# Optimization experiments

Hardware: AMD Instinct MI355X
Metric: run time of the kernel (lower is better)

## Reference

```python
import jax, jax.numpy as jnp
import numpy as np

B, S, H = 128, 1000, 256


def setup_inputs() -> dict:
    key = jax.random.key(0)
    ks = jax.random.split(key, 15)
    sc = 1.0 / np.sqrt(H)
    f = lambda k, shape: (jax.random.normal(k, shape, jnp.float32) * sc)
    return dict(
        static_hidden=jax.random.normal(ks[0], (B, S, H), jnp.float32),
        state_embedding=jax.random.normal(ks[1], (B, 1, H), jnp.float32),
        decoder_hidden=jax.random.normal(ks[2], (B, 1, H), jnp.float32),
        target_hidden=jax.random.normal(ks[3], (B, 1, H), jnp.float32),
        last_hh=jax.random.normal(ks[4], (1, B, H), jnp.float32),
        W_ih=f(ks[5], (3 * H, H)),
        W_hh=f(ks[6], (3 * H, H)),
        b_ih=f(ks[7], (3 * H,)),
        b_hh=f(ks[8], (3 * H,)),
        v_attn_enc=f(ks[9], (H,)),
        W_attn_enc=f(ks[10], (H, 2 * H)),
        v_attn_tgt=f(ks[11], (H,)),
        W_attn_tgt=f(ks[12], (H, 2 * H)),
        v_ptr=f(ks[13], (H,)),
        W_ptr=f(ks[14], (H, 3 * H)),
    )


def _attention(static, dec, v, W):
    # static: [B,S,H], dec: [B,1,H] -> softmax attention over S
    hid = jnp.concatenate([static, jnp.broadcast_to(dec, static.shape)], axis=2)  # [B,S,2H]
    t = jnp.tanh(jnp.einsum('hk,bsk->bhs', W, hid))  # [B,H,S]
    return jax.nn.softmax(jnp.einsum('h,bhs->bs', v, t), axis=1)  # [B,S]


def _gru_step(x, h, Wih, Whh, bih, bhh):
    # single-layer single-step torch GRU semantics; x,h: [B,H]
    gi = x @ Wih.T + bih
    gh = h @ Whh.T + bhh
    ir, iz, ig = jnp.split(gi, 3, axis=-1)
    hr, hz, hg = jnp.split(gh, 3, axis=-1)
    r = jax.nn.sigmoid(ir + hr)
    z = jax.nn.sigmoid(iz + hz)
    n = jnp.tanh(ig + r * hg)
    return (1.0 - z) * n + z * h


def _pointer_branch(static, state_emb, attn, v, W):
    context = jnp.einsum('bs,bsh->bh', attn, static)[:, None, :]  # [B,1,H]
    energy = jnp.concatenate(
        [static,
         jnp.broadcast_to(context, static.shape),
         jnp.broadcast_to(state_emb, static.shape)], axis=2)  # [B,S,3H]
    return jnp.einsum('h,bhs->bs', v, jnp.tanh(jnp.einsum('hk,bsk->bhs', W, energy)))


def reference(static_hidden, state_embedding, decoder_hidden, target_hidden, last_hh,
              W_ih, W_hh, b_ih, b_hh,
              v_attn_enc, W_attn_enc, v_attn_tgt, W_attn_tgt, v_ptr, W_ptr):
    # GRU step (dropout is identity in eval / p=0.0)
    h_new = _gru_step(decoder_hidden[:, 0, :], last_hh[0], W_ih, W_hh, b_ih, b_hh)
    rnn_out = h_new[:, None, :]  # [B,1,H]
    last_hh_new = h_new[None]    # [1,B,H]

    enc_attn = _attention(static_hidden, rnn_out, v_attn_enc, W_attn_enc)
    probs = _pointer_branch(static_hidden, state_embedding, enc_attn, v_ptr, W_ptr)

    tgt_attn = _attention(static_hidden, target_hidden, v_attn_tgt, W_attn_tgt)
    # NOTE: original code reuses self.v / self.W (not v_target/W_taret) for the
    # target branch energy -- replicated faithfully.
    probs_target = _pointer_branch(static_hidden, state_embedding, tgt_attn, v_ptr, W_ptr)

    return (5.0 * probs + probs_target, last_hh_new)
```

## Files before the change

kernel.cpp:

```cpp
#include <hip/hip_runtime.h>
#include <hip/hip_bf16.h>
#include <stdint.h>
#include <stddef.h>

#define Bn 128
#define Sn 1000
#define SP 1024
#define Hn 256

typedef __bf16 bf16;
typedef __bf16 bf16x8 __attribute__((ext_vector_type(8)));
typedef __bf16 bf16x4 __attribute__((ext_vector_type(4)));
typedef __bf16 bf16x2 __attribute__((ext_vector_type(2)));
typedef float  f32x4  __attribute__((ext_vector_type(4)));

typedef __attribute__((address_space(1))) const unsigned int* gas1;
typedef __attribute__((address_space(3))) unsigned int* las3;

__device__ __forceinline__ float fast_tanh(float x){
  return 1.0f - 2.0f / (__expf(2.0f * x) + 1.0f);
}
__device__ __forceinline__ float fast_sigmoid(float x){
  return 1.0f / (1.0f + __expf(-x));
}
__device__ __forceinline__ float dot4(float4 a, float4 b){
  return a.x*b.x + a.y*b.y + a.z*b.z + a.w*b.w;
}

__global__ void k0a_convert(const float* __restrict__ stat, bf16* __restrict__ Abf){
  int p = blockIdx.x * 256 + threadIdx.x;
  int row = p >> 5;
  int ch  = p & 31;
  int s = row & (SP - 1);
  int b = row >> 10;
  float4 f0 = make_float4(0.f,0.f,0.f,0.f), f1 = f0;
  if (s < Sn){
    const float4* src = (const float4*)(stat + ((size_t)(b*Sn + s))*Hn + ch*8);
    f0 = src[0]; f1 = src[1];
  }
  bf16x8 v;
  v[0]=(bf16)f0.x; v[1]=(bf16)f0.y; v[2]=(bf16)f0.z; v[3]=(bf16)f0.w;
  v[4]=(bf16)f1.x; v[5]=(bf16)f1.y; v[6]=(bf16)f1.z; v[7]=(bf16)f1.w;
  *(bf16x8*)(Abf + (size_t)row*Hn + ch*8) = v;
}

__global__ void k0b_weights(const float* __restrict__ We, const float* __restrict__ Wt,
                            const float* __restrict__ Wp, bf16* __restrict__ Wcb,
                            float* __restrict__ sc_e, float* __restrict__ sc_t){
  int t = blockIdx.x * 256 + threadIdx.x;
  if (t < Bn * SP) { sc_e[t] = 0.f; sc_t[t] = 0.f; }
  int r = t >> 8, c = t & 255;
  float val;
  if (r < 256)       val = We[r*512 + c];
  else if (r < 512)  val = Wt[(r-256)*512 + c];
  else               val = Wp[(r-512)*768 + c];
  Wcb[t] = (bf16)val;
}

__global__ void k1_gru(const float* __restrict__ dec, const float* __restrict__ lhh,
                       const float* __restrict__ tgt, const float* __restrict__ se,
                       const float* __restrict__ Wih, const float* __restrict__ Whh,
                       const float* __restrict__ bih, const float* __restrict__ bhh,
                       const float* __restrict__ We,  const float* __restrict__ Wt,
                       const float* __restrict__ Wp,
                       float* __restrict__ out_hh, float* __restrict__ d_enc,
                       float* __restrict__ d_tgt,  float* __restrict__ c3){
  __shared__ __align__(16) float xs[256], hs[256], hn[256], ts[256], ss[256];
  int b = blockIdx.x, t = threadIdx.x;
  xs[t] = dec[b*256 + t];
  hs[t] = lhh[b*256 + t];
  ts[t] = tgt[b*256 + t];
  ss[t] = se[b*256 + t];
  __syncthreads();

  const float4* wir = (const float4*)(Wih + (size_t)t*256);
  const float4* wiz = (const float4*)(Wih + (size_t)(256+t)*256);
  const float4* wig = (const float4*)(Wih + (size_t)(512+t)*256);
  const float4* whr = (const float4*)(Whh + (size_t)t*256);
  const float4* whz = (const float4*)(Whh + (size_t)(256+t)*256);
  const float4* whg = (const float4*)(Whh + (size_t)(512+t)*256);
  float gir=0.f, giz=0.f, gig=0.f, ghr=0.f, ghz=0.f, ghg=0.f;
  #pragma unroll 4
  for (int k=0;k<64;k++){
    float4 xv = ((const float4*)xs)[k];
    float4 hv = ((const float4*)hs)[k];
    gir += dot4(wir[k], xv);
    giz += dot4(wiz[k], xv);
    gig += dot4(wig[k], xv);
    ghr += dot4(whr[k], hv);
    ghz += dot4(whz[k], hv);
    ghg += dot4(whg[k], hv);
  }
  gir += bih[t];      ghr += bhh[t];
  giz += bih[256+t];  ghz += bhh[256+t];
  gig += bih[512+t];  ghg += bhh[512+t];
  float r = fast_sigmoid(gir + ghr);
  float z = fast_sigmoid(giz + ghz);
  float n = fast_tanh(gig + r*ghg);
  float h = (1.f - z)*n + z*hs[t];
  hn[t] = h;
  out_hh[b*256 + t] = h;
  __syncthreads();

  const float4* we2 = (const float4*)(We + (size_t)t*512 + 256);
  const float4* wt2 = (const float4*)(Wt + (size_t)t*512 + 256);
  const float4* wp3 = (const float4*)(Wp + (size_t)t*768 + 512);
  float de=0.f, dt=0.f, cv=0.f;
  #pragma unroll 4
  for (int k=0;k<64;k++){
    float4 hv = ((const float4*)hn)[k];
    float4 tv = ((const float4*)ts)[k];
    float4 sv = ((const float4*)ss)[k];
    de += dot4(we2[k], hv);
    dt += dot4(wt2[k], tv);
    cv += dot4(wp3[k], sv);
  }
  d_enc[b*256 + t] = de;
  d_tgt[b*256 + t] = dt;
  c3[b*256 + t]    = cv;
}

__global__ __launch_bounds__(256) void k2_gemm(
    const bf16* __restrict__ Abf, const bf16* __restrict__ Wcb,
    const float* __restrict__ d_enc, const float* __restrict__ d_tgt,
    const float* __restrict__ c3, const float* __restrict__ v_enc,
    const float* __restrict__ v_tgt,
    float* __restrict__ sc_e, float* __restrict__ sc_t,
    bf16* __restrict__ Aptr){
  __shared__ __align__(16) bf16 As[128*64];
  __shared__ __align__(16) bf16 Bs[128*64];
  int tid = threadIdx.x;
  int w = tid >> 6, l = tid & 63;
  int nc = blockIdx.x, st = blockIdx.y, b = blockIdx.z;
  int wm = (w >> 1) * 64, wn = (w & 1) * 64;
  int lm = l & 15, q = l >> 4;

  const bf16* gA = Abf + (size_t)(b*SP + st*128) * Hn;
  const bf16* gB = Wcb + (size_t)(nc*128) * Hn;
  int srow = w*8 + (l >> 3);
  int scol = (l & 7) * 8;

  f32x4 acc[4][4];
  #pragma unroll
  for (int i=0;i<4;i++)
    #pragma unroll
    for (int j=0;j<4;j++) acc[i][j] = (f32x4){0.f,0.f,0.f,0.f};

  for (int kt=0; kt<4; ++kt){
    __syncthreads();
    #pragma unroll
    for (int r=0;r<4;r++){
      int rowg = r*32 + srow;
      __builtin_amdgcn_global_load_lds((gas1)(gA + (size_t)rowg*Hn + kt*64 + scol),
                                       (las3)(&As[(r*32 + w*8)*64]), 16, 0, 0);
      __builtin_amdgcn_global_load_lds((gas1)(gB + (size_t)rowg*Hn + kt*64 + scol),
                                       (las3)(&Bs[(r*32 + w*8)*64]), 16, 0, 0);
    }
    __syncthreads();
    const bf16* Ab = &As[(wm + lm)*64 + q*8];
    const bf16* Bb = &Bs[(wn + lm)*64 + q*8];
    #pragma unroll
    for (int kk=0; kk<64; kk+=32){
      bf16x8 af[4], bfr[4];
      #pragma unroll
      for (int i=0;i<4;i++) af[i]  = *(const bf16x8*)(Ab + i*16*64 + kk);
      #pragma unroll
      for (int j=0;j<4;j++) bfr[j] = *(const bf16x8*)(Bb + j*16*64 + kk);
      #pragma unroll
      for (int i=0;i<4;i++)
        #pragma unroll
        for (int j=0;j<4;j++)
          acc[i][j] = __builtin_amdgcn_mfma_f32_16x16x32_bf16(af[i], bfr[j], acc[i][j], 0, 0, 0);
    }
  }

  int hb = (nc & 1) * 128;
  if (nc < 4){
    const float* vv = (nc < 2) ? v_enc : v_tgt;
    const float* db = ((nc < 2) ? d_enc : d_tgt) + b*256;
    float* sc = ((nc < 2) ? sc_e : sc_t) + b*SP + st*128;
    float vj[4], dj[4];
    #pragma unroll
    for (int j=0;j<4;j++){
      int hh = hb + wn + j*16 + lm;
      vj[j] = vv[hh]; dj[j] = db[hh];
    }
    #pragma unroll
    for (int i=0;i<4;i++){
      #pragma unroll
      for (int r=0;r<4;r++){
        float p = 0.f;
        #pragma unroll
        for (int j=0;j<4;j++) p += vj[j] * fast_tanh(acc[i][j][r] + dj[j]);
        p += __shfl_xor(p, 1);
        p += __shfl_xor(p, 2);
        p += __shfl_xor(p, 4);
        p += __shfl_xor(p, 8);
        if (lm == 0) atomicAdd(&sc[wm + i*16 + q*4 + r], p);
      }
    }
  } else {
    const float* c3b = c3 + b*256;
    size_t rbase = (size_t)(b*SP + st*128);
    #pragma unroll
    for (int j=0;j<4;j++){
      int hh = hb + wn + j*16 + lm;
      float cv = c3b[hh];
      #pragma unroll
      for (int i=0;i<4;i++){
        #pragma unroll
        for (int r=0;r<4;r++){
          int row = wm + i*16 + q*4 + r;
          Aptr[(rbase + row)*Hn + hh] = (bf16)(acc[i][j][r] + cv);
        }
      }
    }
  }
}

__global__ void k3_softmax_ctx(const float* __restrict__ sc_e, const float* __restrict__ sc_t,
                               const bf16* __restrict__ Abf, const float* __restrict__ Wp,
                               float* __restrict__ c2e, float* __restrict__ c2t){
  int b = blockIdx.x, which = blockIdx.y, t = threadIdx.x;
  const float* sc = which ? sc_t : sc_e;
  float* c2 = which ? c2t : c2e;
  __shared__ __align__(16) float at[Sn];
  __shared__ float red[256];
  __shared__ __align__(16) float ctx[256];
  __shared__ float2 partc[2][128];

  float lmax = -1e30f;
  #pragma unroll
  for (int i=0;i<4;i++){
    int s = t + i*256;
    if (s < Sn){ float v = sc[b*SP + s]; at[s] = v; lmax = fmaxf(lmax, v); }
  }
  red[t] = lmax; __syncthreads();
  for (int o=128;o>0;o>>=1){ if (t < o) red[t] = fmaxf(red[t], red[t+o]); __syncthreads(); }
  float mx = red[0]; __syncthreads();

  float lsum = 0.f;
  #pragma unroll
  for (int i=0;i<4;i++){
    int s = t + i*256;
    if (s < Sn){ float e = __expf(at[s] - mx); at[s] = e; lsum += e; }
  }
  red[t] = lsum; __syncthreads();
  for (int o=128;o>0;o>>=1){ if (t < o) red[t] += red[t+o]; __syncthreads(); }
  float inv = 1.0f / red[0];
  #pragma unroll
  for (int i=0;i<4;i++){
    int s = t + i*256;
    if (s < Sn) at[s] *= inv;
  }
  __syncthreads();

  int hp = t & 127, sh = t >> 7;
  float a0 = 0.f, a1 = 0.f;
  const bf16* base = Abf + ((size_t)(b*SP + sh*500))*Hn + hp*2;
  #pragma unroll 4
  for (int s2=0; s2<500; s2++){
    float wgt = at[sh*500 + s2];
    bf16x2 pr = *(const bf16x2*)(base + (size_t)s2*Hn);
    a0 += wgt * (float)pr[0];
    a1 += wgt * (float)pr[1];
  }
  partc[sh][hp] = make_float2(a0, a1);
  __syncthreads();
  if (t < 128){
    float2 p0 = partc[0][t], p1 = partc[1][t];
    ctx[2*t]   = p0.x + p1.x;
    ctx[2*t+1] = p0.y + p1.y;
  }
  __syncthreads();

  const float4* wrow = (const float4*)(Wp + (size_t)t*768 + 256);
  float acc = 0.f;
  #pragma unroll 4
  for (int k=0;k<64;k++) acc += dot4(wrow[k], ((const float4*)ctx)[k]);
  c2[b*256 + t] = acc;
}

__global__ void k4_final(const bf16* __restrict__ Aptr, const float* __restrict__ c2e,
                         const float* __restrict__ c2t, const float* __restrict__ vp,
                         float* __restrict__ out){
  int w = threadIdx.x >> 6, l = threadIdx.x & 63;
  int row = blockIdx.x*4 + w;
  int b = row / 1000;
  int s = row - b*1000;
  const bf16* ap = Aptr + ((size_t)(b*SP + s))*Hn + l*4;
  bf16x4 av = *(const bf16x4*)ap;
  float4 ce = *(const float4*)(c2e + b*256 + l*4);
  float4 ct = *(const float4*)(c2t + b*256 + l*4);
  float4 vv = *(const float4*)(vp + l*4);
  float a0 = (float)av[0], a1 = (float)av[1], a2 = (float)av[2], a3 = (float)av[3];
  float pe = vv.x*fast_tanh(a0+ce.x) + vv.y*fast_tanh(a1+ce.y)
           + vv.z*fast_tanh(a2+ce.z) + vv.w*fast_tanh(a3+ce.w);
  float pt = vv.x*fast_tanh(a0+ct.x) + vv.y*fast_tanh(a1+ct.y)
           + vv.z*fast_tanh(a2+ct.z) + vv.w*fast_tanh(a3+ct.w);
  #pragma unroll
  for (int o=1;o<64;o<<=1){
    pe += __shfl_xor(pe, o);
    pt += __shfl_xor(pt, o);
  }
  if (l == 0) out[row] = 5.0f*pe + pt;
}

extern "C" void kernel_launch(void* const* d_in, const int* in_sizes, int n_in,
                              void* d_out, int out_size, void* d_ws, size_t ws_size,
                              hipStream_t stream){
  const float* stat = (const float*)d_in[0];
  const float* se   = (const float*)d_in[1];
  const float* dec  = (const float*)d_in[2];
  const float* tgt  = (const float*)d_in[3];
  const float* lhh  = (const float*)d_in[4];
  const float* Wih  = (const float*)d_in[5];
  const float* Whh  = (const float*)d_in[6];
  const float* bih  = (const float*)d_in[7];
  const float* bhh  = (const float*)d_in[8];
  const float* vEnc = (const float*)d_in[9];
  const float* WEnc = (const float*)d_in[10];
  const float* vTgt = (const float*)d_in[11];
  const float* WTgt = (const float*)d_in[12];
  const float* vPtr = (const float*)d_in[13];
  const float* WPtr = (const float*)d_in[14];
  float* out = (float*)d_out;

  char* wsp = (char*)d_ws;
  bf16*  Abf  = (bf16*)(wsp);
  bf16*  Aptr = (bf16*)(wsp + 67108864);
  bf16*  Wcb  = (bf16*)(wsp + 134217728);
  float* scE  = (float*)(wsp + 134610944);
  float* scT  = (float*)(wsp + 135135232);
  float* dEnc = (float*)(wsp + 135659520);
  float* dTgt = (float*)(wsp + 135790592);
  float* c3   = (float*)(wsp + 135921664);
  float* c2e  = (float*)(wsp + 136052736);
  float* c2t  = (float*)(wsp + 136183808);

  hipLaunchKernelGGL(k0a_convert, dim3(16384), dim3(256), 0, stream, stat, Abf);
  hipLaunchKernelGGL(k0b_weights, dim3(768), dim3(256), 0, stream,
                     WEnc, WTgt, WPtr, Wcb, scE, scT);
  hipLaunchKernelGGL(k1_gru, dim3(128), dim3(256), 0, stream,
                     dec, lhh, tgt, se, Wih, Whh, bih, bhh, WEnc, WTgt, WPtr,
                     out + Bn*Sn, dEnc, dTgt, c3);
  hipLaunchKernelGGL(k2_gemm, dim3(6, 8, 128), dim3(256), 0, stream,
                     Abf, Wcb, dEnc, dTgt, c3, vEnc, vTgt, scE, scT, Aptr);
  hipLaunchKernelGGL(k3_softmax_ctx, dim3(128, 2), dim3(256), 0, stream,
                     scE, scT, Abf, WPtr, c2e, c2t);
  hipLaunchKernelGGL(k4_final, dim3(32000), dim3(256), 0, stream,
                     Aptr, c2e, c2t, vPtr, out);
}
```

Baseline: 511.2 us.

## Keep A tile resident across all weight chunks and split softmax-context kernel

```diff
diff --git a/kernel.cpp b/kernel.cpp
--- a/kernel.cpp
+++ b/kernel.cpp
@@ -45,10 +45,8 @@
 }
 
 __global__ void k0b_weights(const float* __restrict__ We, const float* __restrict__ Wt,
-                            const float* __restrict__ Wp, bf16* __restrict__ Wcb,
-                            float* __restrict__ sc_e, float* __restrict__ sc_t){
+                            const float* __restrict__ Wp, bf16* __restrict__ Wcb){
   int t = blockIdx.x * 256 + threadIdx.x;
-  if (t < Bn * SP) { sc_e[t] = 0.f; sc_t[t] = 0.f; }
   int r = t >> 8, c = t & 255;
   float val;
   if (r < 256)       val = We[r*512 + c];
@@ -127,158 +125,210 @@
     const float* __restrict__ v_tgt,
     float* __restrict__ sc_e, float* __restrict__ sc_t,
     bf16* __restrict__ Aptr){
-  __shared__ __align__(16) bf16 As[128*64];
+  __shared__ __align__(16) bf16 As[64*256];
   __shared__ __align__(16) bf16 Bs[128*64];
+  __shared__ float scoreE[64], scoreT[64];
   int tid = threadIdx.x;
   int w = tid >> 6, l = tid & 63;
-  int nc = blockIdx.x, st = blockIdx.y, b = blockIdx.z;
-  int wm = (w >> 1) * 64, wn = (w & 1) * 64;
+  int st = blockIdx.x, b = blockIdx.y;
+  int wm = (w & 1) * 32, wn = (w >> 1) * 64;
   int lm = l & 15, q = l >> 4;
 
-  const bf16* gA = Abf + (size_t)(b*SP + st*128) * Hn;
-  const bf16* gB = Wcb + (size_t)(nc*128) * Hn;
-  int srow = w*8 + (l >> 3);
-  int scol = (l & 7) * 8;
-
-  f32x4 acc[4][4];
-  #pragma unroll
-  for (int i=0;i<4;i++)
+  if (tid < 64) scoreE[tid] = 0.f;
+  else if (tid < 128) scoreT[tid-64] = 0.f;
+
+  {
+    const bf16* gA = Abf + ((size_t)(b*SP + st*64)) * Hn;
+    int rl = w*2 + (l >> 5);
+    int ch = l & 31;
     #pragma unroll
-    for (int j=0;j<4;j++) acc[i][j] = (f32x4){0.f,0.f,0.f,0.f};
-
-  for (int kt=0; kt<4; ++kt){
-    __syncthreads();
+    for (int is = 0; is < 8; is++){
+      int row = is*8 + rl;
+      int sc_ = ch ^ (row & 7);
+      __builtin_amdgcn_global_load_lds((gas1)(gA + (size_t)row*256 + sc_*8),
+                                       (las3)(&As[(is*8 + w*2)*256]), 16, 0, 0);
+    }
+  }
+
+  int rB8 = w*8 + (l >> 3);
+  int chB = l & 7;
+
+  for (int nc = 0; nc < 6; nc++){
+    f32x4 acc[2][4];
     #pragma unroll
-    for (int r=0;r<4;r++){
-      int rowg = r*32 + srow;
-      __builtin_amdgcn_global_load_lds((gas1)(gA + (size_t)rowg*Hn + kt*64 + scol),
-                                       (las3)(&As[(r*32 + w*8)*64]), 16, 0, 0);
-      __builtin_amdgcn_global_load_lds((gas1)(gB + (size_t)rowg*Hn + kt*64 + scol),
-                                       (las3)(&Bs[(r*32 + w*8)*64]), 16, 0, 0);
+    for (int i=0;i<2;i++)
+      #pragma unroll
+      for (int j=0;j<4;j++) acc[i][j] = (f32x4){0.f,0.f,0.f,0.f};
+
+    for (int kt = 0; kt < 4; kt++){
+      __syncthreads();
+      #pragma unroll
+      for (int is = 0; is < 4; is++){
+        int row = is*32 + rB8;
+        int sc_ = chB ^ (row & 7);
+        __builtin_amdgcn_global_load_lds((gas1)(Wcb + ((size_t)(nc*128 + row))*256 + kt*64 + sc_*8),
+                                         (las3)(&Bs[(is*32 + w*8)*64]), 16, 0, 0);
+      }
+      __syncthreads();
+      #pragma unroll
+      for (int kk = 0; kk < 64; kk += 32){
+        bf16x8 af[2], bfr[4];
+        int cA = kt*8 + (kk >> 3) + q;
+        int cB = (kk >> 3) + q;
+        #pragma unroll
+        for (int i=0;i<2;i++){
+          int rA = wm + i*16 + lm;
+          af[i] = *(const bf16x8*)(&As[rA*256 + ((cA ^ (rA & 7)) << 3)]);
+        }
+        #pragma unroll
+        for (int j=0;j<4;j++){
+          int rB = wn + j*16 + lm;
+          bfr[j] = *(const bf16x8*)(&Bs[rB*64 + ((cB ^ (rB & 7)) << 3)]);
+        }
+        #pragma unroll
+        for (int i=0;i<2;i++)
+          #pragma unroll
+          for (int j=0;j<4;j++)
+            acc[i][j] = __builtin_amdgcn_mfma_f32_16x16x32_bf16(af[i], bfr[j], acc[i][j], 0, 0, 0);
+      }
     }
-    __syncthreads();
-    const bf16* Ab = &As[(wm + lm)*64 + q*8];
-    const bf16* Bb = &Bs[(wn + lm)*64 + q*8];
-    #pragma unroll
-    for (int kk=0; kk<64; kk+=32){
-      bf16x8 af[4], bfr[4];
-      #pragma unroll
-      for (int i=0;i<4;i++) af[i]  = *(const bf16x8*)(Ab + i*16*64 + kk);
-      #pragma unroll
-      for (int j=0;j<4;j++) bfr[j] = *(const bf16x8*)(Bb + j*16*64 + kk);
-      #pragma unroll
-      for (int i=0;i<4;i++)
+
+    int hb = (nc & 1) * 128;
+    if (nc < 4){
+      const float* vv = (nc < 2) ? v_enc : v_tgt;
+      const float* db = ((nc < 2) ? d_enc : d_tgt) + b*256;
+      float* sc = (nc < 2) ? scoreE : scoreT;
+      float vj[4], dj[4];
+      #pragma unroll
+      for (int j=0;j<4;j++){
+        int hh = hb + wn + j*16 + lm;
+        vj[j] = vv[hh]; dj[j] = db[hh];
+      }
+      #pragma unroll
+      for (int i=0;i<2;i++){
         #pragma unroll
-        for (int j=0;j<4;j++)
-          acc[i][j] = __builtin_amdgcn_mfma_f32_16x16x32_bf16(af[i], bfr[j], acc[i][j], 0, 0, 0);
-    }
-  }
-
-  int hb = (nc & 1) * 128;
-  if (nc < 4){
-    const float* vv = (nc < 2) ? v_enc : v_tgt;
-    const float* db = ((nc < 2) ? d_enc : d_tgt) + b*256;
-    float* sc = ((nc < 2) ? sc_e : sc_t) + b*SP + st*128;
-    float vj[4], dj[4];
-    #pragma unroll
-    for (int j=0;j<4;j++){
-      int hh = hb + wn + j*16 + lm;
-      vj[j] = vv[hh]; dj[j] = db[hh];
-    }
-    #pragma unroll
-    for (int i=0;i<4;i++){
-      #pragma unroll
-      for (int r=0;r<4;r++){
-        float p = 0.f;
-        #pragma unroll
-        for (int j=0;j<4;j++) p += vj[j] * fast_tanh(acc[i][j][r] + dj[j]);
-        p += __shfl_xor(p, 1);
-        p += __shfl_xor(p, 2);
-        p += __shfl_xor(p, 4);
-        p += __shfl_xor(p, 8);
-        if (lm == 0) atomicAdd(&sc[wm + i*16 + q*4 + r], p);
-      }
-    }
-  } else {
-    const float* c3b = c3 + b*256;
-    size_t rbase = (size_t)(b*SP + st*128);
-    #pragma unroll
-    for (int j=0;j<4;j++){
-      int hh = hb + wn + j*16 + lm;
-      float cv = c3b[hh];
-      #pragma unroll
-      for (int i=0;i<4;i++){
+        for (int r=0;r<4;r++){
+          float p = 0.f;
+          #pragma unroll
+          for (int j=0;j<4;j++) p += vj[j] * fast_tanh(acc[i][j][r] + dj[j]);
+          p += __shfl_xor(p, 1);
+          p += __shfl_xor(p, 2);
+          p += __shfl_xor(p, 4);
+          p += __shfl_xor(p, 8);
+          if (lm == 0) atomicAdd(&sc[wm + i*16 + q*4 + r], p);
+        }
+      }
+    } else {
+      int hbp = (nc - 4) * 128;
+      const float* c3b = c3 + b*256;
+      float cv[4]; int hhj[4];
+      #pragma unroll
+      for (int j=0;j<4;j++){
+        hhj[j] = hbp + wn + j*16 + lm;
+        cv[j] = c3b[hhj[j]];
+      }
+      #pragma unroll
+      for (int i=0;i<2;i++){
         #pragma unroll
         for (int r=0;r<4;r++){
           int row = wm + i*16 + q*4 + r;
-          Aptr[(rbase + row)*Hn + hh] = (bf16)(acc[i][j][r] + cv);
+          int gs = st*64 + row;
+          if (gs < Sn){
+            size_t rb = ((size_t)(b*Sn + gs))*256;
+            #pragma unroll
+            for (int j=0;j<4;j++)
+              Aptr[rb + hhj[j]] = (bf16)(acc[i][j][r] + cv[j]);
+          }
         }
       }
     }
   }
-}
-
-__global__ void k3_softmax_ctx(const float* __restrict__ sc_e, const float* __restrict__ sc_t,
-                               const bf16* __restrict__ Abf, const float* __restrict__ Wp,
-                               float* __restrict__ c2e, float* __restrict__ c2t){
+
+  __syncthreads();
+  if (tid < 64)       sc_e[b*SP + st*64 + tid]      = scoreE[tid];
+  else if (tid < 128) sc_t[b*SP + st*64 + tid - 64] = scoreT[tid-64];
+}
+
+__global__ __launch_bounds__(1024) void k3_ctx(
+    const float* __restrict__ sc_e, const float* __restrict__ sc_t,
+    const bf16* __restrict__ Abf,
+    float* __restrict__ ctxPE, float* __restrict__ ctxPT){
+  __shared__ float attE[1024], attT[1024];
+  __shared__ float redE[16], redT[16];
+  __shared__ float pe[8*256], pt[8*256];
+  int b = blockIdx.x, sp = blockIdx.y, t = threadIdx.x;
+  int wid = t >> 6, ln = t & 63;
+
+  float vE = (t < Sn) ? sc_e[b*SP + t] : -1e30f;
+  float vT = (t < Sn) ? sc_t[b*SP + t] : -1e30f;
+  float mE = vE, mT = vT;
+  #pragma unroll
+  for (int o=1;o<64;o<<=1){ mE = fmaxf(mE, __shfl_xor(mE,o)); mT = fmaxf(mT, __shfl_xor(mT,o)); }
+  if (ln == 0){ redE[wid] = mE; redT[wid] = mT; }
+  __syncthreads();
+  float ME = -1e30f, MT = -1e30f;
+  #pragma unroll
+  for (int i=0;i<16;i++){ ME = fmaxf(ME, redE[i]); MT = fmaxf(MT, redT[i]); }
+  __syncthreads();
+  float eE = (t < Sn) ? __expf(vE - ME) : 0.f;
+  float eT = (t < Sn) ? __expf(vT - MT) : 0.f;
+  float sE = eE, sT = eT;
+  #pragma unroll
+  for (int o=1;o<64;o<<=1){ sE += __shfl_xor(sE,o); sT += __shfl_xor(sT,o); }
+  if (ln == 0){ redE[wid] = sE; redT[wid] = sT; }
+  __syncthreads();
+  float SE = 0.f, ST = 0.f;
+  #pragma unroll
+  for (int i=0;i<16;i++){ SE += redE[i]; ST += redT[i]; }
+  attE[t] = eE / SE;
+  attT[t] = eT / ST;
+  __syncthreads();
+
+  int sh = t >> 7, hp = t & 127;
+  const bf16* base = Abf + ((size_t)(b*SP + sp*500))*Hn + hp*2;
+  float aE0=0.f, aE1=0.f, aT0=0.f, aT1=0.f;
+  #pragma unroll 4
+  for (int i=0;i<63;i++){
+    int sl = sh + 8*i;
+    if (sl < 500){
+      int s = sp*500 + sl;
+      float wE = attE[s], wT = attT[s];
+      bf16x2 pr = *(const bf16x2*)(base + (size_t)sl*Hn);
+      float p0 = (float)pr[0], p1 = (float)pr[1];
+      aE0 += wE*p0; aE1 += wE*p1;
+      aT0 += wT*p0; aT1 += wT*p1;
+    }
+  }
+  pe[sh*256 + hp*2] = aE0; pe[sh*256 + hp*2+1] = aE1;
+  pt[sh*256 + hp*2] = aT0; pt[sh*256 + hp*2+1] = aT1;
+  __syncthreads();
+  if (t < 256){
+    float s = 0.f;
+    #pragma unroll
+    for (int i=0;i<8;i++) s += pe[i*256 + t];
+    ctxPE[((size_t)(sp*Bn + b))*256 + t] = s;
+  } else if (t < 512){
+    int tt = t - 256;
+    float s = 0.f;
+    #pragma unroll
+    for (int i=0;i<8;i++) s += pt[i*256 + tt];
+    ctxPT[((size_t)(sp*Bn + b))*256 + tt] = s;
+  }
+}
+
+__global__ void k3c_c2(const float* __restrict__ ctxPE, const float* __restrict__ ctxPT,
+                       const float* __restrict__ Wp,
+                       float* __restrict__ c2e, float* __restrict__ c2t){
+  __shared__ __align__(16) float ctx[256];
   int b = blockIdx.x, which = blockIdx.y, t = threadIdx.x;
-  const float* sc = which ? sc_t : sc_e;
-  float* c2 = which ? c2t : c2e;
-  __shared__ __align__(16) float at[Sn];
-  __shared__ float red[256];
-  __shared__ __align__(16) float ctx[256];
-  __shared__ float2 partc[2][128];
-
-  float lmax = -1e30f;
-  #pragma unroll
-  for (int i=0;i<4;i++){
-    int s = t + i*256;
-    if (s < Sn){ float v = sc[b*SP + s]; at[s] = v; lmax = fmaxf(lmax, v); }
-  }
-  red[t] = lmax; __syncthreads();
-  for (int o=128;o>0;o>>=1){ if (t < o) red[t] = fmaxf(red[t], red[t+o]); __syncthreads(); }
-  float mx = red[0]; __syncthreads();
-
-  float lsum = 0.f;
-  #pragma unroll
-  for (int i=0;i<4;i++){
-    int s = t + i*256;
-    if (s < Sn){ float e = __expf(at[s] - mx); at[s] = e; lsum += e; }
-  }
-  red[t] = lsum; __syncthreads();
-  for (int o=128;o>0;o>>=1){ if (t < o) red[t] += red[t+o]; __syncthreads(); }
-  float inv = 1.0f / red[0];
-  #pragma unroll
-  for (int i=0;i<4;i++){
-    int s = t + i*256;
-    if (s < Sn) at[s] *= inv;
-  }
-  __syncthreads();
-
-  int hp = t & 127, sh = t >> 7;
-  float a0 = 0.f, a1 = 0.f;
-  const bf16* base = Abf + ((size_t)(b*SP + sh*500))*Hn + hp*2;
-  #pragma unroll 4
-  for (int s2=0; s2<500; s2++){
-    float wgt = at[sh*500 + s2];
-    bf16x2 pr = *(const bf16x2*)(base + (size_t)s2*Hn);
-    a0 += wgt * (float)pr[0];
-    a1 += wgt * (float)pr[1];
-  }
-  partc[sh][hp] = make_float2(a0, a1);
-  __syncthreads();
-  if (t < 128){
-    float2 p0 = partc[0][t], p1 = partc[1][t];
-    ctx[2*t]   = p0.x + p1.x;
-    ctx[2*t+1] = p0.y + p1.y;
-  }
-  __syncthreads();
-
+  const float* cp = which ? ctxPT : ctxPE;
+  ctx[t] = cp[(size_t)b*256 + t] + cp[((size_t)(Bn + b))*256 + t];
+  __syncthreads();
   const float4* wrow = (const float4*)(Wp + (size_t)t*768 + 256);
   float acc = 0.f;
   #pragma unroll 4
   for (int k=0;k<64;k++) acc += dot4(wrow[k], ((const float4*)ctx)[k]);
-  c2[b*256 + t] = acc;
+  (which ? c2t : c2e)[b*256 + t] = acc;
 }
 
 __global__ void k4_final(const bf16* __restrict__ Aptr, const float* __restrict__ c2e,
@@ -287,8 +337,7 @@
   int w = threadIdx.x >> 6, l = threadIdx.x & 63;
   int row = blockIdx.x*4 + w;
   int b = row / 1000;
-  int s = row - b*1000;
-  const bf16* ap = Aptr + ((size_t)(b*SP + s))*Hn + l*4;
+  const bf16* ap = Aptr + (size_t)row*Hn + l*4;
   bf16x4 av = *(const bf16x4*)ap;
   float4 ce = *(const float4*)(c2e + b*256 + l*4);
   float4 ct = *(const float4*)(c2t + b*256 + l*4);
@@ -329,25 +378,28 @@
   char* wsp = (char*)d_ws;
   bf16*  Abf  = (bf16*)(wsp);
   bf16*  Aptr = (bf16*)(wsp + 67108864);
-  bf16*  Wcb  = (bf16*)(wsp + 134217728);
-  float* scE  = (float*)(wsp + 134610944);
-  float* scT  = (float*)(wsp + 135135232);
-  float* dEnc = (float*)(wsp + 135659520);
-  float* dTgt = (float*)(wsp + 135790592);
-  float* c3   = (float*)(wsp + 135921664);
-  float* c2e  = (float*)(wsp + 136052736);
-  float* c2t  = (float*)(wsp + 136183808);
+  bf16*  Wcb  = (bf16*)(wsp + 132644864);
+  float* scE  = (float*)(wsp + 133038080);
+  float* scT  = (float*)(wsp + 133562368);
+  float* dEnc = (float*)(wsp + 134086656);
+  float* dTgt = (float*)(wsp + 134217728);
+  float* c3   = (float*)(wsp + 134348800);
+  float* c2e  = (float*)(wsp + 134479872);
+  float* c2t  = (float*)(wsp + 134610944);
+  float* ctxPE= (float*)(wsp + 134742016);
+  float* ctxPT= (float*)(wsp + 135004160);
 
   hipLaunchKernelGGL(k0a_convert, dim3(16384), dim3(256), 0, stream, stat, Abf);
-  hipLaunchKernelGGL(k0b_weights, dim3(768), dim3(256), 0, stream,
-                     WEnc, WTgt, WPtr, Wcb, scE, scT);
+  hipLaunchKernelGGL(k0b_weights, dim3(768), dim3(256), 0, stream, WEnc, WTgt, WPtr, Wcb);
   hipLaunchKernelGGL(k1_gru, dim3(128), dim3(256), 0, stream,
                      dec, lhh, tgt, se, Wih, Whh, bih, bhh, WEnc, WTgt, WPtr,
                      out + Bn*Sn, dEnc, dTgt, c3);
-  hipLaunchKernelGGL(k2_gemm, dim3(6, 8, 128), dim3(256), 0, stream,
+  hipLaunchKernelGGL(k2_gemm, dim3(16, 128), dim3(256), 0, stream,
                      Abf, Wcb, dEnc, dTgt, c3, vEnc, vTgt, scE, scT, Aptr);
-  hipLaunchKernelGGL(k3_softmax_ctx, dim3(128, 2), dim3(256), 0, stream,
-                     scE, scT, Abf, WPtr, c2e, c2t);
+  hipLaunchKernelGGL(k3_ctx, dim3(128, 2), dim3(1024), 0, stream,
+                     scE, scT, Abf, ctxPE, ctxPT);
+  hipLaunchKernelGGL(k3c_c2, dim3(128, 2), dim3(256), 0, stream,
+                     ctxPE, ctxPT, WPtr, c2e, c2t);
   hipLaunchKernelGGL(k4_final, dim3(32000), dim3(256), 0, stream,
                      Aptr, c2e, c2t, vPtr, out);
 }
```

Measured after the change: 464.1 us. 1.1x faster.
